# Kernel tuning notes

Hardware: AMD Instinct MI355X
Metric: run time of the kernel (lower is better)

## Reference

```python
import jax, jax.numpy as jnp
import numpy as np

C = 16          # scalar multiplicity of Rs_hidden = [(16, 0)]
NB = 10         # number_of_basis
H = 12          # radial MLP hidden size
MAX_R = 10.0
CENTERS = jnp.linspace(0.0, MAX_R, NB)
SIGMA = 0.8 * (MAX_R / (NB - 1))
GAUSS_NORM = 1.423085244900308   # e3nn GaussianRadialModel basis normalizer
Y0 = 1.0 / (2.0 * np.sqrt(np.pi))  # Y_{l=0} spherical harmonic constant


def setup_inputs() -> dict:
    key = jax.random.key(0)
    ks = jax.random.split(key, 9)
    z, n1, n2 = 4, 192, 192
    return {
        'input1': jax.random.normal(ks[0], (z, n1, C), jnp.float32),
        'input2': jax.random.normal(ks[1], (z, n2, C), jnp.float32),
        'xyz1': jax.random.normal(ks[2], (z, n1, 3), jnp.float32),
        'xyz2': jax.random.normal(ks[3], (z, n2, 3), jnp.float32),
        'mask': jax.random.randint(ks[4], (z, n1 + n2), 0, 2),
        'W_rad1': jax.random.normal(ks[5], (NB, H), jnp.float32),
        'W_rad_out': jax.random.normal(ks[6], (H, C * C), jnp.float32),
        'W_fc3': jax.random.normal(ks[7], (C, C), jnp.float32),
        'W_fc2': jax.random.normal(ks[8], (C, 1), jnp.float32),
    }


def _normalize(x, eps=1e-6):
    # torch .std defaults to unbiased (ddof=1)
    mean = x.mean(-1, keepdims=True)
    std = jnp.std(x, axis=-1, keepdims=True, ddof=1)
    return (x - mean) / (std + eps)


def reference(input1, input2, xyz1, xyz2, mask, W_rad1, W_rad_out, W_fc3, W_fc2):
    x = jnp.concatenate([input1, input2], axis=1)    # [z, n, C]
    xyz = jnp.concatenate([xyz1, xyz2], axis=1)      # [z, n, 3]
    z, n = x.shape[0], x.shape[1]

    # pairwise distances (eps keeps sqrt grad finite on the diagonal)
    diff = xyz[:, :, None, :] - xyz[:, None, :, :]   # [z, n, n, 3]
    d = jnp.sqrt(jnp.sum(diff * diff, axis=-1) + 1e-12)  # [z, n, n]

    # Gaussian radial basis + weight-normalized FC radial model (swish act)
    basis = jnp.exp(-jnp.square((d[..., None] - CENTERS) / SIGMA)) / GAUSS_NORM  # [z,n,n,NB]
    hmid = jax.nn.silu(basis @ W_rad1 / np.sqrt(NB))          # [z, n, n, H]
    R = hmid @ W_rad_out / np.sqrt(H)                         # [z, n, n, C*C]

    # l=0 TFN kernel: radial weights * Y_0 (trivial Clebsch-Gordan for scalars)
    K = R.reshape(z, n, n, C, C) * Y0                         # [z, a, b, i, j]
    y = jnp.einsum('zabij,zbj->zai', K, x)                    # [z, n, C]

    # Norm(Rs_hidden): per-irrep L2 norm; for scalars it's |x|
    y = jnp.abs(y)
    y = jnp.where(mask[..., None] == 0, 0.0, y)

    s = _normalize(jnp.sum(y, axis=1))                        # [z, C]
    h3 = jax.nn.leaky_relu(s @ W_fc3 / np.sqrt(C))            # fc3 + leaky_relu
    o = h3 @ W_fc2 / np.sqrt(C)                               # fc2
    return jax.nn.sigmoid(o).reshape(-1)                      # [z]
```

## Files before the change

### kernel.cpp

```cpp
#include <hip/hip_runtime.h>
#include <math.h>

#define Z     4
#define N1    192
#define NN    384
#define C     16
#define NB    10
#define H     12
#define ATILE 4
#define NAT   (NN / ATILE)
#define SPLIT 3

__device__ __forceinline__ float3 load_xyz(const float* __restrict__ xyz1,
                                           const float* __restrict__ xyz2,
                                           int z, int node) {
    const float* p = (node < N1) ? (xyz1 + (z * N1 + node) * 3)
                                 : (xyz2 + (z * N1 + (node - N1)) * 3);
    return make_float3(p[0], p[1], p[2]);
}

__global__ void k1_precompute_T(const float* __restrict__ in1,
                                const float* __restrict__ in2,
                                const float* __restrict__ Wro,
                                float* __restrict__ T) {
    const int bid = blockIdx.x;
    const int z = bid / NN, b = bid % NN;
    const int t = threadIdx.x;

    __shared__ float xl[C];
    if (t < C) {
        const float* xp = (b < N1) ? (in1 + (z * N1 + b) * C)
                                   : (in2 + (z * N1 + (b - N1)) * C);
        xl[t] = xp[t];
    }
    __syncthreads();

    const int h = t >> 4, i = t & 15;
    const float* w = Wro + h * (C * C) + i * C;
    float acc = 0.0f;
    #pragma unroll
    for (int j = 0; j < C; ++j) acc += w[j] * xl[j];

    const float scale = 0.28209479177387814f * 0.2886751345948129f;
    T[bid * (H * C) + t] = acc * scale;
}

__global__ __launch_bounds__(128) void k2_pairs(const float* __restrict__ xyz1,
                                                const float* __restrict__ xyz2,
                                                const float* __restrict__ Wr1,
                                                const float* __restrict__ T,
                                                float* __restrict__ partial) {
    const int bid = blockIdx.x;
    const int sp  = bid % SPLIT;
    const int za  = bid / SPLIT;
    const int z   = za / NAT, at = za % NAT;
    const int a0  = at * ATILE;
    const int tid = threadIdx.x;
    const int lane = tid & 63, wv = tid >> 6;
    const int b = sp * 128 + tid;

    __shared__ float W1s[NB * H];
    __shared__ float red[2][64];
    if (tid < NB * H) W1s[tid] = Wr1[tid] * 0.31622776601683794f;
    __syncthreads();

    const float3 pb = load_xyz(xyz1, xyz2, z, b);

    float v[ATILE * C];
    #pragma unroll
    for (int p = 0; p < ATILE * C; ++p) v[p] = 0.0f;

    const float invSigma = 1.125f;
    const float invGN    = 0.7027283689263438f;
    const float4* tp = (const float4*)(T + (z * NN + b) * (H * C));

    #pragma unroll
    for (int pass = 0; pass < 2; ++pass) {
        float hm[2][H];
        #pragma unroll
        for (int aa = 0; aa < 2; ++aa) {
            const int a = a0 + pass * 2 + aa;
            const float3 pa = load_xyz(xyz1, xyz2, z, a);
            const float dx = pa.x - pb.x, dy = pa.y - pb.y, dz = pa.z - pb.z;
            const float d = sqrtf(dx * dx + dy * dy + dz * dz + 1e-12f);

            float basis[NB];
            #pragma unroll
            for (int k = 0; k < NB; ++k) {
                const float u = (d - (float)k * (10.0f / 9.0f)) * invSigma;
                basis[k] = __expf(-u * u) * invGN;
            }
            #pragma unroll
            for (int h = 0; h < H; ++h) {
                float acc = 0.0f;
                #pragma unroll
                for (int k = 0; k < NB; ++k) acc += basis[k] * W1s[k * H + h];
                hm[aa][h] = acc / (1.0f + __expf(-acc));
            }
        }

        #pragma unroll
        for (int h = 0; h < H; ++h) {
            const float4 t0 = tp[h * 4 + 0];
            const float4 t1 = tp[h * 4 + 1];
            const float4 t2 = tp[h * 4 + 2];
            const float4 t3 = tp[h * 4 + 3];
            #pragma unroll
            for (int aa = 0; aa < 2; ++aa) {
                const float f = hm[aa][h];
                const int o = (pass * 2 + aa) * C;
                v[o +  0] += f * t0.x;  v[o +  1] += f * t0.y;
                v[o +  2] += f * t0.z;  v[o +  3] += f * t0.w;
                v[o +  4] += f * t1.x;  v[o +  5] += f * t1.y;
                v[o +  6] += f * t1.z;  v[o +  7] += f * t1.w;
                v[o +  8] += f * t2.x;  v[o +  9] += f * t2.y;
                v[o + 10] += f * t2.z;  v[o + 11] += f * t2.w;
                v[o + 12] += f * t3.x;  v[o + 13] += f * t3.y;
                v[o + 14] += f * t3.z;  v[o + 15] += f * t3.w;
            }
        }
    }

    #pragma unroll
    for (int k = 0; k < 6; ++k) {
        const int m = 32 >> k;
        const int bsel = (lane >> k) & 1;
        #pragma unroll
        for (int j = 0; j < m; ++j) {
            const float lo = v[j], hi = v[m + j];
            const float sendv = bsel ? lo : hi;
            const float recv = __shfl_xor(sendv, 1 << k, 64);
            v[j] = (bsel ? hi : lo) + recv;
        }
    }
    const int l = lane;
    const int pos = ((l & 1) << 5) | ((l & 2) << 3) | ((l & 4) << 1) |
                    ((l & 8) >> 1) | ((l & 16) >> 3) | ((l & 32) >> 5);
    red[wv][pos] = v[0];
    __syncthreads();
    if (tid < 64) partial[bid * 64 + tid] = red[0][tid] + red[1][tid];
}

__global__ __launch_bounds__(256) void k3_head(const float* __restrict__ partial,
                                               const int* __restrict__ mask,
                                               const float* __restrict__ Wfc3,
                                               const float* __restrict__ Wfc2,
                                               float* __restrict__ out) {
    const int z = blockIdx.x;
    const int t = threadIdx.x;
    const int i = t & 15, ch = t >> 4;

    __shared__ float red[16][17];
    __shared__ float sv[C];

    float acc = 0.0f;
    #pragma unroll
    for (int r = 0; r < 24; ++r) {
        const int a  = ch * 24 + r;
        const int at = a >> 2, t2 = a & 3;
        const int base = ((z * NAT + at) * SPLIT) * 64 + t2 * 16 + i;
        float val = partial[base] + partial[base + 64] + partial[base + 128];
        val = fabsf(val);
        if (mask[z * NN + a] != 0) acc += val;
    }
    red[ch][i] = acc;
    __syncthreads();
    if (t < C) {
        float s = 0.0f;
        #pragma unroll
        for (int c2 = 0; c2 < 16; ++c2) s += red[c2][t];
        sv[t] = s;
    }
    __syncthreads();

    if (t == 0) {
        float v[C];
        float mean = 0.0f;
        #pragma unroll
        for (int q = 0; q < C; ++q) { v[q] = sv[q]; mean += v[q]; }
        mean *= (1.0f / C);
        float var = 0.0f;
        #pragma unroll
        for (int q = 0; q < C; ++q) { const float d = v[q] - mean; var += d * d; }
        const float sd = sqrtf(var / (float)(C - 1)) + 1e-6f;
        #pragma unroll
        for (int q = 0; q < C; ++q) v[q] = (v[q] - mean) / sd;

        float o = 0.0f;
        #pragma unroll
        for (int k = 0; k < C; ++k) {
            float h3 = 0.0f;
            #pragma unroll
            for (int q = 0; q < C; ++q) h3 += v[q] * Wfc3[q * C + k];
            h3 *= 0.25f;
            h3 = (h3 > 0.0f) ? h3 : 0.01f * h3;
            o += h3 * Wfc2[k];
        }
        o *= 0.25f;
        out[z] = 1.0f / (1.0f + __expf(-o));
    }
}

extern "C" void kernel_launch(void* const* d_in, const int* in_sizes, int n_in,
                              void* d_out, int out_size, void* d_ws, size_t ws_size,
                              hipStream_t stream) {
    const float* in1  = (const float*)d_in[0];
    const float* in2  = (const float*)d_in[1];
    const float* xyz1 = (const float*)d_in[2];
    const float* xyz2 = (const float*)d_in[3];
    const int*   mask = (const int*)d_in[4];
    const float* Wr1  = (const float*)d_in[5];
    const float* Wro  = (const float*)d_in[6];
    const float* Wfc3 = (const float*)d_in[7];
    const float* Wfc2 = (const float*)d_in[8];
    float* out = (float*)d_out;

    float* T       = (float*)d_ws;
    float* partial = T + Z * NN * H * C;

    k1_precompute_T<<<Z * NN, 192, 0, stream>>>(in1, in2, Wro, T);
    k2_pairs<<<Z * NAT * SPLIT, 128, 0, stream>>>(xyz1, xyz2, Wr1, T, partial);
    k3_head<<<Z, 256, 0, stream>>>(partial, mask, Wfc3, Wfc2, out);
}
```

Baseline: 103.5 us.

## Split output channels across waves and double b-split in pair kernel

Each block now covers 64 b nodes instead of 128, and its two waves split the 16 output channels (8 each) rather than the b range. SPLIT doubles to 6, so the grid grows. The radial MLP is computed for all 4 a-nodes up front with fused basis accumulation and a folded normalizer, and launch bounds request 4 blocks per CU. The aim is fewer registers per thread and more blocks for occupancy. In exchange, each wave recomputes the distance, basis and MLP work, and k3 reads twice as many partials.

Measured after the change: 115.7 us. +11.7%, slower.

```diff
diff --git a/kernel.cpp b/kernel.cpp
--- a/kernel.cpp
+++ b/kernel.cpp
@@ -9,7 +9,7 @@
 #define H     12
 #define ATILE 4
 #define NAT   (NN / ATILE)
-#define SPLIT 3
+#define SPLIT 6
 
 __device__ __forceinline__ float3 load_xyz(const float* __restrict__ xyz1,
                                            const float* __restrict__ xyz2,
@@ -45,11 +45,11 @@
     T[bid * (H * C) + t] = acc * scale;
 }
 
-__global__ __launch_bounds__(128) void k2_pairs(const float* __restrict__ xyz1,
-                                                const float* __restrict__ xyz2,
-                                                const float* __restrict__ Wr1,
-                                                const float* __restrict__ T,
-                                                float* __restrict__ partial) {
+__global__ __launch_bounds__(128, 4) void k2_pairs(const float* __restrict__ xyz1,
+                                                   const float* __restrict__ xyz2,
+                                                   const float* __restrict__ Wr1,
+                                                   const float* __restrict__ T,
+                                                   float* __restrict__ partial) {
     const int bid = blockIdx.x;
     const int sp  = bid % SPLIT;
     const int za  = bid / SPLIT;
@@ -57,73 +57,62 @@
     const int a0  = at * ATILE;
     const int tid = threadIdx.x;
     const int lane = tid & 63, wv = tid >> 6;
-    const int b = sp * 128 + tid;
+    const int b = sp * 64 + lane;
 
     __shared__ float W1s[NB * H];
-    __shared__ float red[2][64];
-    if (tid < NB * H) W1s[tid] = Wr1[tid] * 0.31622776601683794f;
+    __shared__ float red[2][32];
+    if (tid < NB * H)
+        W1s[tid] = Wr1[tid] * (0.31622776601683794f * 0.7027283689263438f);
     __syncthreads();
 
     const float3 pb = load_xyz(xyz1, xyz2, z, b);
-
-    float v[ATILE * C];
-    #pragma unroll
-    for (int p = 0; p < ATILE * C; ++p) v[p] = 0.0f;
-
     const float invSigma = 1.125f;
-    const float invGN    = 0.7027283689263438f;
-    const float4* tp = (const float4*)(T + (z * NN + b) * (H * C));
-
-    #pragma unroll
-    for (int pass = 0; pass < 2; ++pass) {
-        float hm[2][H];
-        #pragma unroll
-        for (int aa = 0; aa < 2; ++aa) {
-            const int a = a0 + pass * 2 + aa;
-            const float3 pa = load_xyz(xyz1, xyz2, z, a);
-            const float dx = pa.x - pb.x, dy = pa.y - pb.y, dz = pa.z - pb.z;
-            const float d = sqrtf(dx * dx + dy * dy + dz * dz + 1e-12f);
-
-            float basis[NB];
+
+    float hm[ATILE][H];
+    #pragma unroll
+    for (int aa = 0; aa < ATILE; ++aa) {
+        const float3 pa = load_xyz(xyz1, xyz2, z, a0 + aa);
+        const float dx = pa.x - pb.x, dy = pa.y - pb.y, dz = pa.z - pb.z;
+        const float d = sqrtf(dx * dx + dy * dy + dz * dz + 1e-12f);
+
+        float acc[H];
+        #pragma unroll
+        for (int h = 0; h < H; ++h) acc[h] = 0.0f;
+        #pragma unroll
+        for (int k = 0; k < NB; ++k) {
+            const float u = (d - (float)k * (10.0f / 9.0f)) * invSigma;
+            const float e = __expf(-u * u);
             #pragma unroll
-            for (int k = 0; k < NB; ++k) {
-                const float u = (d - (float)k * (10.0f / 9.0f)) * invSigma;
-                basis[k] = __expf(-u * u) * invGN;
-            }
-            #pragma unroll
-            for (int h = 0; h < H; ++h) {
-                float acc = 0.0f;
-                #pragma unroll
-                for (int k = 0; k < NB; ++k) acc += basis[k] * W1s[k * H + h];
-                hm[aa][h] = acc / (1.0f + __expf(-acc));
-            }
-        }
-
-        #pragma unroll
-        for (int h = 0; h < H; ++h) {
-            const float4 t0 = tp[h * 4 + 0];
-            const float4 t1 = tp[h * 4 + 1];
-            const float4 t2 = tp[h * 4 + 2];
-            const float4 t3 = tp[h * 4 + 3];
-            #pragma unroll
-            for (int aa = 0; aa < 2; ++aa) {
-                const float f = hm[aa][h];
-                const int o = (pass * 2 + aa) * C;
-                v[o +  0] += f * t0.x;  v[o +  1] += f * t0.y;
-                v[o +  2] += f * t0.z;  v[o +  3] += f * t0.w;
-                v[o +  4] += f * t1.x;  v[o +  5] += f * t1.y;
-                v[o +  6] += f * t1.z;  v[o +  7] += f * t1.w;
-                v[o +  8] += f * t2.x;  v[o +  9] += f * t2.y;
-                v[o + 10] += f * t2.z;  v[o + 11] += f * t2.w;
-                v[o + 12] += f * t3.x;  v[o + 13] += f * t3.y;
-                v[o + 14] += f * t3.z;  v[o + 15] += f * t3.w;
-            }
-        }
-    }
-
-    #pragma unroll
-    for (int k = 0; k < 6; ++k) {
-        const int m = 32 >> k;
+            for (int h = 0; h < H; ++h) acc[h] += e * W1s[k * H + h];
+        }
+        #pragma unroll
+        for (int h = 0; h < H; ++h)
+            hm[aa][h] = acc[h] / (1.0f + __expf(-acc[h]));
+    }
+
+    float v[ATILE * 8];
+    #pragma unroll
+    for (int p = 0; p < ATILE * 8; ++p) v[p] = 0.0f;
+
+    const float4* tp = (const float4*)(T + (z * NN + b) * (H * C)) + wv * 2;
+    #pragma unroll
+    for (int h = 0; h < H; ++h) {
+        const float4 t0 = tp[h * 4 + 0];
+        const float4 t1 = tp[h * 4 + 1];
+        #pragma unroll
+        for (int aa = 0; aa < ATILE; ++aa) {
+            const float f = hm[aa][h];
+            const int o = aa * 8;
+            v[o + 0] += f * t0.x;  v[o + 1] += f * t0.y;
+            v[o + 2] += f * t0.z;  v[o + 3] += f * t0.w;
+            v[o + 4] += f * t1.x;  v[o + 5] += f * t1.y;
+            v[o + 6] += f * t1.z;  v[o + 7] += f * t1.w;
+        }
+    }
+
+    #pragma unroll
+    for (int k = 0; k < 5; ++k) {
+        const int m = 16 >> k;
         const int bsel = (lane >> k) & 1;
         #pragma unroll
         for (int j = 0; j < m; ++j) {
@@ -133,12 +122,22 @@
             v[j] = (bsel ? hi : lo) + recv;
         }
     }
-    const int l = lane;
-    const int pos = ((l & 1) << 5) | ((l & 2) << 3) | ((l & 4) << 1) |
-                    ((l & 8) >> 1) | ((l & 16) >> 3) | ((l & 32) >> 5);
-    red[wv][pos] = v[0];
-    __syncthreads();
-    if (tid < 64) partial[bid * 64 + tid] = red[0][tid] + red[1][tid];
+    {
+        const float recv = __shfl_xor(v[0], 32, 64);
+        v[0] += recv;
+    }
+    const int l = lane & 31;
+    const int pos = ((l & 1) << 4) | ((l & 2) << 2) | (l & 4) |
+                    ((l & 8) >> 2) | ((l & 16) >> 4);
+    if (lane < 32) red[wv][pos] = v[0];
+    __syncthreads();
+
+    if (tid < 64) {
+        const int a_off = tid >> 4, i = tid & 15;
+        const float val = (i < 8) ? red[0][a_off * 8 + i]
+                                  : red[1][a_off * 8 + (i - 8)];
+        partial[bid * 64 + tid] = val;
+    }
 }
 
 __global__ __launch_bounds__(256) void k3_head(const float* __restrict__ partial,
@@ -159,7 +158,9 @@
         const int a  = ch * 24 + r;
         const int at = a >> 2, t2 = a & 3;
         const int base = ((z * NAT + at) * SPLIT) * 64 + t2 * 16 + i;
-        float val = partial[base] + partial[base + 64] + partial[base + 128];
+        float val = 0.0f;
+        #pragma unroll
+        for (int s = 0; s < SPLIT; ++s) val += partial[base + s * 64];
         val = fabsf(val);
         if (mask[z * NN + a] != 0) acc += val;
     }
```
